# Kernel tuning notes

Hardware: AMD Instinct MI355X
Metric: run time of the kernel (lower is better)

Reference implementation:

```python
import jax, jax.numpy as jnp
import numpy as np

NUM_NODES = 20000
NUM_EDGES = 65536
WIDTH = 64
EDGE_FEAT = 6
HIDDEN = 128


def setup_inputs() -> dict:
    key = jax.random.key(0)
    ks = jax.random.split(key, 6)
    x = jax.random.normal(ks[0], (NUM_NODES, WIDTH), dtype=jnp.float32)
    edge_attr = jax.random.normal(ks[1], (NUM_EDGES, EDGE_FEAT), dtype=jnp.float32)
    # weight-generating MLP params (the `nn` callable), fan-in scaled
    W1 = jax.random.normal(ks[2], (EDGE_FEAT, HIDDEN), dtype=jnp.float32) / np.sqrt(EDGE_FEAT)
    b1 = jnp.zeros((HIDDEN,), dtype=jnp.float32)
    W2 = jax.random.normal(ks[3], (HIDDEN, WIDTH * WIDTH), dtype=jnp.float32) / np.sqrt(HIDDEN)
    b2 = jnp.zeros((WIDTH * WIDTH,), dtype=jnp.float32)
    senders = jax.random.randint(ks[4], (NUM_EDGES,), 0, NUM_NODES)
    receivers = jax.random.randint(ks[5], (NUM_EDGES,), 0, NUM_NODES)
    return {"x": x, "edge_attr": edge_attr, "W1": W1, "b1": b1,
            "W2": W2, "b2": b2, "senders": senders, "receivers": receivers}


def reference(x, edge_attr, W1, b1, W2, b2, senders, receivers):
    n_segs, width = x.shape
    # nn(edge_attr): (E, width*width) edge-conditioned weights
    h = jax.nn.relu(edge_attr @ W1 + b1)
    weight = (h @ W2 + b2).reshape(-1, width, width)  # (E, w, w)
    # gather sender features, per-edge (1,w) @ (w,w) matmul -> (E, w)
    msgs = jnp.einsum('ew,ewv->ev', x[senders], weight)
    # scatter-sum messages into receiver nodes (aggr == 'sum')
    return jax.ops.segment_sum(msgs, receivers, num_segments=n_segs)
```

## Files before the change

### kernel.cpp

```cpp
#include <hip/hip_runtime.h>
#include <stdint.h>

typedef _Float16 f16;
typedef f16 f16x8 __attribute__((ext_vector_type(8)));
typedef float f32x4 __attribute__((ext_vector_type(4)));

#define NUM_NODES 20000
#define NUM_EDGES 65536
#define WIDTH 64
#define EDGE_FEAT 6
#define HIDDEN 128
#define BM 256
#define NCHUNK 129
#define XPAD 72

#define XH_HALFS (NUM_NODES * WIDTH)
#define XCONV_BLKS 625
#define ZOUT_BLKS 625

__global__ __launch_bounds__(256) void prep_kernel(
    const float* __restrict__ x, const float* __restrict__ W2,
    const float* __restrict__ b2, f16* __restrict__ ws_h,
    float* __restrict__ out)
{
  __shared__ float row[4096];
  f16* x_h = ws_h;
  f16* W2g = ws_h + XH_HALFS;
  const int blk = blockIdx.x, tid = threadIdx.x;

  if (blk < NCHUNK) {
    const int ki = blk;
    const float* srcrow;
    if (ki < HIDDEN) {
      const float4* src = (const float4*)(W2 + (size_t)ki * 4096);
      #pragma unroll
      for (int i = 0; i < 4; ++i) {
        float4 v = src[tid + 256 * i];
        *(float4*)&row[(tid + 256 * i) * 4] = v;
      }
      __syncthreads();
      srcrow = row;
    } else {
      srcrow = b2;
    }
    const int obase = tid * 16;
    f16x8 outv0, outv1;
    #pragma unroll
    for (int u = 0; u < 8; ++u) {
      int o = obase + u;
      int n = o >> 6, pg = (o >> 3) & 7, j = o & 7;
      int k = (pg ^ (n & 7)) * 8 + j;
      outv0[u] = (f16)srcrow[k * 64 + n];
    }
    #pragma unroll
    for (int u = 0; u < 8; ++u) {
      int o = obase + 8 + u;
      int n = o >> 6, pg = (o >> 3) & 7, j = o & 7;
      int k = (pg ^ (n & 7)) * 8 + j;
      outv1[u] = (f16)srcrow[k * 64 + n];
    }
    *(f16x8*)&W2g[(size_t)ki * 4096 + obase] = outv0;
    *(f16x8*)&W2g[(size_t)ki * 4096 + obase + 8] = outv1;
  } else if (blk < NCHUNK + XCONV_BLKS) {
    int idx = (blk - NCHUNK) * 2048 + tid * 8;
    if (idx + 8 <= XH_HALFS) {
      float4 a = *(const float4*)(x + idx);
      float4 b = *(const float4*)(x + idx + 4);
      f16x8 hv;
      hv[0] = (f16)a.x; hv[1] = (f16)a.y; hv[2] = (f16)a.z; hv[3] = (f16)a.w;
      hv[4] = (f16)b.x; hv[5] = (f16)b.y; hv[6] = (f16)b.z; hv[7] = (f16)b.w;
      *(f16x8*)&x_h[idx] = hv;
    }
  } else {
    int idx = (blk - NCHUNK - XCONV_BLKS) * 2048 + tid * 8;
    float4 z = {0.f, 0.f, 0.f, 0.f};
    *(float4*)(out + idx) = z;
    *(float4*)(out + idx + 4) = z;
  }
}

__global__ __launch_bounds__(256, 2) void nnconv_kernel(
    const float* __restrict__ ea, const float* __restrict__ W1,
    const float* __restrict__ b1, const int* __restrict__ senders,
    const int* __restrict__ receivers, const f16* __restrict__ ws_h,
    float* __restrict__ out)
{
  const f16* x_h = ws_h;
  const f16* W2g = ws_h + XH_HALFS;
  __shared__ __align__(16) f16 xt[BM][XPAD];
  __shared__ __align__(16) f16 Bb[2][4096];

  const int tid = threadIdx.x;
  const int lane = tid & 63, wid = tid >> 6;
  const int quad = lane >> 4, l15 = lane & 15;
  const int chunk = blockIdx.x & 255;
  const int khalf = blockIdx.x >> 8;
  const int k0 = khalf ? 65 : 0;
  const int kcount = khalf ? 64 : 65;
  const int e0 = chunk * BM;
  const int rowbase = wid * 64;

  {
    int s = senders[e0 + tid];
    const uint4* src = (const uint4*)(x_h + (size_t)s * WIDTH);
    uint4* dst = (uint4*)&xt[tid][0];
    #pragma unroll
    for (int i = 0; i < 8; ++i) dst[i] = src[i];
  }

  float ear[4][6];
  #pragma unroll
  for (int t = 0; t < 4; ++t) {
    const float* p = ea + (size_t)(e0 + rowbase + t * 16 + l15) * EDGE_FEAT;
    #pragma unroll
    for (int f = 0; f < 6; ++f) ear[t][f] = p[f];
  }

  int boff[2][4];
  #pragma unroll
  for (int kc = 0; kc < 2; ++kc)
    #pragma unroll
    for (int nt = 0; nt < 4; ++nt) {
      int n = nt * 16 + l15;
      int g = kc * 4 + quad;
      boff[kc][nt] = n * 64 + (g ^ (n & 7)) * 8;
    }

  uint4 pre0 = *(const uint4*)(W2g + (size_t)k0 * 4096 + tid * 8);
  uint4 pre1 = *(const uint4*)(W2g + (size_t)k0 * 4096 + 2048 + tid * 8);

  __syncthreads();

  f16x8 xf[4][2];
  #pragma unroll
  for (int t = 0; t < 4; ++t)
    #pragma unroll
    for (int kc = 0; kc < 2; ++kc)
      xf[t][kc] = *(const f16x8*)&xt[rowbase + t * 16 + l15][kc * 32 + quad * 8];

  f32x4 acc[4][4];
  #pragma unroll
  for (int t = 0; t < 4; ++t)
    #pragma unroll
    for (int nt = 0; nt < 4; ++nt)
      acc[t][nt] = (f32x4){0.f, 0.f, 0.f, 0.f};

  for (int kk = 0; kk < kcount; ++kk) {
    const int ki = k0 + kk;
    f16* buf = &Bb[kk & 1][0];
    *(uint4*)&buf[tid * 8] = pre0;
    *(uint4*)&buf[2048 + tid * 8] = pre1;

    f16 hv[4];
    if (ki < HIDDEN) {
      float b1c = b1[ki];
      float w1c[6];
      #pragma unroll
      for (int f = 0; f < 6; ++f) w1c[f] = W1[f * HIDDEN + ki];
      #pragma unroll
      for (int t = 0; t < 4; ++t) {
        float s = b1c;
        #pragma unroll
        for (int f = 0; f < 6; ++f) s = fmaf(ear[t][f], w1c[f], s);
        hv[t] = (f16)fmaxf(s, 0.f);
      }
    } else {
      #pragma unroll
      for (int t = 0; t < 4; ++t) hv[t] = (f16)1.f;
    }

    __syncthreads();

    if (kk + 1 < kcount) {
      pre0 = *(const uint4*)(W2g + (size_t)(ki + 1) * 4096 + tid * 8);
      pre1 = *(const uint4*)(W2g + (size_t)(ki + 1) * 4096 + 2048 + tid * 8);
    }

    f16x8 bf[2][4];
    #pragma unroll
    for (int kc = 0; kc < 2; ++kc)
      #pragma unroll
      for (int nt = 0; nt < 4; ++nt)
        bf[kc][nt] = *(const f16x8*)&buf[boff[kc][nt]];

    #pragma unroll
    for (int t = 0; t < 4; ++t) {
      f16x8 sa0 = xf[t][0] * hv[t];
      f16x8 sa1 = xf[t][1] * hv[t];
      #pragma unroll
      for (int nt = 0; nt < 4; ++nt) {
        acc[t][nt] = __builtin_amdgcn_mfma_f32_16x16x32_f16(sa0, bf[0][nt], acc[t][nt], 0, 0, 0);
        acc[t][nt] = __builtin_amdgcn_mfma_f32_16x16x32_f16(sa1, bf[1][nt], acc[t][nt], 0, 0, 0);
      }
    }
  }

  #pragma unroll
  for (int t = 0; t < 4; ++t) {
    int ebase = e0 + rowbase + t * 16 + quad * 4;
    int rc[4];
    #pragma unroll
    for (int r = 0; r < 4; ++r) rc[r] = receivers[ebase + r];
    #pragma unroll
    for (int nt = 0; nt < 4; ++nt) {
      int v = nt * 16 + l15;
      #pragma unroll
      for (int r = 0; r < 4; ++r)
        atomicAdd(out + (size_t)rc[r] * WIDTH + v, acc[t][nt][r]);
    }
  }
}

extern "C" void kernel_launch(void* const* d_in, const int* in_sizes, int n_in,
                              void* d_out, int out_size, void* d_ws, size_t ws_size,
                              hipStream_t stream) {
  const float* x  = (const float*)d_in[0];
  const float* ea = (const float*)d_in[1];
  const float* W1 = (const float*)d_in[2];
  const float* b1 = (const float*)d_in[3];
  const float* W2 = (const float*)d_in[4];
  const float* b2 = (const float*)d_in[5];
  const int* snd  = (const int*)d_in[6];
  const int* rcv  = (const int*)d_in[7];
  float* out = (float*)d_out;
  f16* wsh = (f16*)d_ws;

  prep_kernel<<<NCHUNK + XCONV_BLKS + ZOUT_BLKS, 256, 0, stream>>>(x, W2, b2, wsh, out);
  nnconv_kernel<<<2 * (NUM_EDGES / BM), 256, 0, stream>>>(ea, W1, b1, snd, rcv, wsh, out);
}
```

Measured before the change: 153.2 us.

## Load W2 fragments directly from global into registers, dropping LDS staging

The prep kernel now writes W2 as a plain transpose without the XOR swizzle. The main loop loads each wave's B fragments straight from global/L2 into registers, double-buffered across an unrolled pair of steps, instead of staging through shared memory. This removes the LDS stores and loads and the per-iteration __syncthreads. In exchange every wave fetches the full 4096-half slice itself, which quadruples global/L2 traffic for W2 and raises register pressure.

```diff
diff --git a/kernel.cpp b/kernel.cpp
--- a/kernel.cpp
+++ b/kernel.cpp
@@ -48,16 +48,12 @@
     #pragma unroll
     for (int u = 0; u < 8; ++u) {
       int o = obase + u;
-      int n = o >> 6, pg = (o >> 3) & 7, j = o & 7;
-      int k = (pg ^ (n & 7)) * 8 + j;
-      outv0[u] = (f16)srcrow[k * 64 + n];
+      outv0[u] = (f16)srcrow[(o & 63) * 64 + (o >> 6)];
     }
     #pragma unroll
     for (int u = 0; u < 8; ++u) {
       int o = obase + 8 + u;
-      int n = o >> 6, pg = (o >> 3) & 7, j = o & 7;
-      int k = (pg ^ (n & 7)) * 8 + j;
-      outv1[u] = (f16)srcrow[k * 64 + n];
+      outv1[u] = (f16)srcrow[(o & 63) * 64 + (o >> 6)];
     }
     *(f16x8*)&W2g[(size_t)ki * 4096 + obase] = outv0;
     *(f16x8*)&W2g[(size_t)ki * 4096 + obase + 8] = outv1;
@@ -88,7 +84,6 @@
   const f16* x_h = ws_h;
   const f16* W2g = ws_h + XH_HALFS;
   __shared__ __align__(16) f16 xt[BM][XPAD];
-  __shared__ __align__(16) f16 Bb[2][4096];
 
   const int tid = threadIdx.x;
   const int lane = tid & 63, wid = tid >> 6;
@@ -116,18 +111,15 @@
     for (int f = 0; f < 6; ++f) ear[t][f] = p[f];
   }
 
-  int boff[2][4];
+  const int goff0 = l15 * 64 + quad * 8;
+
+  const f16* wp = W2g + (size_t)k0 * 4096;
+  f16x8 bfA[8], bfB[8];
   #pragma unroll
   for (int kc = 0; kc < 2; ++kc)
     #pragma unroll
-    for (int nt = 0; nt < 4; ++nt) {
-      int n = nt * 16 + l15;
-      int g = kc * 4 + quad;
-      boff[kc][nt] = n * 64 + (g ^ (n & 7)) * 8;
-    }
-
-  uint4 pre0 = *(const uint4*)(W2g + (size_t)k0 * 4096 + tid * 8);
-  uint4 pre1 = *(const uint4*)(W2g + (size_t)k0 * 4096 + 2048 + tid * 8);
+    for (int nt = 0; nt < 4; ++nt)
+      bfA[kc * 4 + nt] = *(const f16x8*)(wp + goff0 + nt * 1024 + kc * 32);
 
   __syncthreads();
 
@@ -145,55 +137,61 @@
     for (int nt = 0; nt < 4; ++nt)
       acc[t][nt] = (f32x4){0.f, 0.f, 0.f, 0.f};
 
-  for (int kk = 0; kk < kcount; ++kk) {
-    const int ki = k0 + kk;
-    f16* buf = &Bb[kk & 1][0];
-    *(uint4*)&buf[tid * 8] = pre0;
-    *(uint4*)&buf[2048 + tid * 8] = pre1;
-
-    f16 hv[4];
-    if (ki < HIDDEN) {
-      float b1c = b1[ki];
-      float w1c[6];
-      #pragma unroll
-      for (int f = 0; f < 6; ++f) w1c[f] = W1[f * HIDDEN + ki];
-      #pragma unroll
-      for (int t = 0; t < 4; ++t) {
-        float s = b1c;
-        #pragma unroll
-        for (int f = 0; f < 6; ++f) s = fmaf(ear[t][f], w1c[f], s);
-        hv[t] = (f16)fmaxf(s, 0.f);
-      }
-    } else {
-      #pragma unroll
-      for (int t = 0; t < 4; ++t) hv[t] = (f16)1.f;
-    }
-
-    __syncthreads();
-
-    if (kk + 1 < kcount) {
-      pre0 = *(const uint4*)(W2g + (size_t)(ki + 1) * 4096 + tid * 8);
-      pre1 = *(const uint4*)(W2g + (size_t)(ki + 1) * 4096 + 2048 + tid * 8);
-    }
-
-    f16x8 bf[2][4];
-    #pragma unroll
-    for (int kc = 0; kc < 2; ++kc)
-      #pragma unroll
-      for (int nt = 0; nt < 4; ++nt)
-        bf[kc][nt] = *(const f16x8*)&buf[boff[kc][nt]];
-
-    #pragma unroll
-    for (int t = 0; t < 4; ++t) {
-      f16x8 sa0 = xf[t][0] * hv[t];
-      f16x8 sa1 = xf[t][1] * hv[t];
-      #pragma unroll
-      for (int nt = 0; nt < 4; ++nt) {
-        acc[t][nt] = __builtin_amdgcn_mfma_f32_16x16x32_f16(sa0, bf[0][nt], acc[t][nt], 0, 0, 0);
-        acc[t][nt] = __builtin_amdgcn_mfma_f32_16x16x32_f16(sa1, bf[1][nt], acc[t][nt], 0, 0, 0);
-      }
-    }
-  }
+  int ki = k0;
+
+#define STEP(BCUR, BNXT, PREF)                                              \
+  {                                                                         \
+    if (PREF) {                                                             \
+      const f16* wpn = wp + 4096;                                           \
+      _Pragma("unroll")                                                     \
+      for (int kc = 0; kc < 2; ++kc)                                        \
+        _Pragma("unroll")                                                   \
+        for (int nt = 0; nt < 4; ++nt)                                      \
+          BNXT[kc * 4 + nt] =                                               \
+              *(const f16x8*)(wpn + goff0 + nt * 1024 + kc * 32);           \
+    }                                                                       \
+    f16 hv[4];                                                              \
+    if (ki < HIDDEN) {                                                      \
+      float b1c = b1[ki];                                                   \
+      float w1c[6];                                                         \
+      _Pragma("unroll")                                                     \
+      for (int f = 0; f < 6; ++f) w1c[f] = W1[f * HIDDEN + ki];             \
+      _Pragma("unroll")                                                     \
+      for (int t = 0; t < 4; ++t) {                                         \
+        float s = b1c;                                                      \
+        _Pragma("unroll")                                                   \
+        for (int f = 0; f < 6; ++f) s = fmaf(ear[t][f], w1c[f], s);         \
+        hv[t] = (f16)fmaxf(s, 0.f);                                        \
+      }                                                                     \
+    } else {                                                                \
+      _Pragma("unroll")                                                     \
+      for (int t = 0; t < 4; ++t) hv[t] = (f16)1.f;                         \
+    }                                                                       \
+    _Pragma("unroll")                                                       \
+    for (int t = 0; t < 4; ++t) {                                           \
+      f16x8 sa0 = xf[t][0] * hv[t];                                         \
+      f16x8 sa1 = xf[t][1] * hv[t];                                         \
+      _Pragma("unroll")                                                     \
+      for (int nt = 0; nt < 4; ++nt) {                                      \
+        acc[t][nt] = __builtin_amdgcn_mfma_f32_16x16x32_f16(                \
+            sa0, BCUR[nt], acc[t][nt], 0, 0, 0);                            \
+        acc[t][nt] = __builtin_amdgcn_mfma_f32_16x16x32_f16(                \
+            sa1, BCUR[4 + nt], acc[t][nt], 0, 0, 0);                        \
+      }                                                                     \
+    }                                                                       \
+    wp += 4096;                                                             \
+    ++ki;                                                                   \
+  }
+
+  int kk = 0;
+  for (; kk + 2 <= kcount; kk += 2) {
+    STEP(bfA, bfB, true);
+    STEP(bfB, bfA, (kk + 2 < kcount));
+  }
+  if (kk < kcount) {
+    STEP(bfA, bfB, false);
+  }
+#undef STEP
 
   #pragma unroll
   for (int t = 0; t < 4; ++t) {
```

Measured after the change: 205.1 us. 1.34x slower.
